# Kernel tuning notes

Hardware: AMD Instinct MI355X
Metric: run time of the kernel (lower is better)

Reference implementation:

```python
import jax, jax.numpy as jnp
import numpy as np
import math

LOG2PI = math.log(2.0 * math.pi)
NEG = -1e20


def gaussian_loglik(z, mean, log_std):
    tmp = (z - mean) * jnp.exp(-log_std)
    return -0.5 * (tmp * tmp + 2.0 * log_std + LOG2PI)


def setup_inputs() -> dict:
    key = jax.random.key(0)
    k1, k2 = jax.random.split(key)
    N, T, D = 16, 2048, 2
    # event arrival times, increasing along T
    input_time = jnp.sort(jax.random.uniform(k1, (N, T, 1), dtype=jnp.float32), axis=1)
    input_loc = jax.random.normal(k2, (N, T, D), dtype=jnp.float32)
    return {
        "input_time": input_time,
        "input_loc": input_loc,
        "mu0": jnp.asarray(0.0, jnp.float32),
        "logstd0": jnp.asarray(0.0, jnp.float32),
        "coeff_decay": jnp.asarray(0.1, jnp.float32),
        "spatial_logstd": jnp.asarray(0.1, jnp.float32),
    }


def reference(input_time, input_loc, mu0, logstd0, coeff_decay, spatial_logstd):
    N, T, _ = input_time.shape
    # base log-likelihood of the first event location under N(mu0, exp(logstd0))
    s0 = input_loc[:, 0]                                   # (N, D)
    loglik0 = gaussian_loglik(s0, mu0, logstd0).sum(-1)    # (N,)

    # pairwise time differences dt[n,i,j] = t[n,i] - t[n,j]
    dt = input_time - jnp.swapaxes(input_time, 1, 2)       # (N, T, T)

    # pairwise spatial Gaussian log-likelihoods, summed over D
    pw = gaussian_loglik(
        input_loc[:, :, None, :],                          # (N, T, 1, D)
        input_loc[:, None, :, :],                          # (N, 1, T, D)
        spatial_logstd,
    ).sum(-1)                                              # (N, T, T)

    # causal mask: keep strictly-lower triangle, fill rest with -1e20
    mask = jnp.tril(jnp.ones((T, T), dtype=bool), k=-1)
    pw = jnp.where(mask, pw, NEG)

    dt_logdecay = jnp.where(mask, -dt / jax.nn.softplus(coeff_decay), NEG)
    dt_logdecay = dt_logdecay - jax.nn.logsumexp(dt_logdecay, axis=-1, keepdims=True)

    loglik = jax.nn.logsumexp(pw + dt_logdecay, axis=-1)   # (N, T)
    return jnp.concatenate([loglik0[:, None], loglik[:, 1:]], axis=1)
```

## Files before the change

kernel.cpp:

```cpp
#include <hip/hip_runtime.h>
#include <math.h>

#define TT     2048
#define LOG2E  1.4426950408889634f
#define LN2    0.6931471805599453f
#define LOG2PI 1.8378770664093453f

__global__ __launch_bounds__(256) void gmsm_scan(
    const float* __restrict__ time,
    const float* __restrict__ loc,
    const float* __restrict__ coeffp,
    const float* __restrict__ lsp,
    float4* __restrict__ packed)
{
    const int n    = blockIdx.x;
    const int tid  = threadIdx.x;
    const int lane = tid & 63;
    const int wv   = tid >> 6;

    const float sp = log1pf(expf(*coeffp));
    const float ss = LOG2E / sp;
    const float ls = *lsp;
    const float c1 = -0.5f * expf(-2.0f * ls) * LOG2E;
    const float c0 = -(2.0f * ls + LOG2PI);

    const float4* tp = (const float4*)(time + (size_t)n * TT);
    const float4* lp = (const float4*)(loc  + (size_t)n * TT * 2);
    float4* pk = packed + (size_t)n * TT;

    const float4 t0 = tp[tid * 2 + 0];
    const float4 t1 = tp[tid * 2 + 1];
    const float4 l0 = lp[tid * 4 + 0];
    const float4 l1 = lp[tid * 4 + 1];
    const float4 l2 = lp[tid * 4 + 2];
    const float4 l3 = lp[tid * 4 + 3];

    const float tt[8] = {t0.x, t0.y, t0.z, t0.w, t1.x, t1.y, t1.z, t1.w};
    const float xx[8] = {l0.x, l0.z, l1.x, l1.z, l2.x, l2.z, l3.x, l3.z};
    const float yy[8] = {l0.y, l0.w, l1.y, l1.w, l2.y, l2.w, l3.y, l3.w};

    float bt[8], P[8];
    float run = 0.0f;
    #pragma unroll
    for (int k = 0; k < 8; ++k) {
        bt[k] = tt[k] * ss;
        run += __builtin_amdgcn_exp2f(bt[k]);
        P[k] = run;
    }
    const float tot = run;

    float v = tot;
    #pragma unroll
    for (int d = 1; d < 64; d <<= 1) {
        const float o = __shfl_up(v, d, 64);
        if (lane >= d) v += o;
    }
    __shared__ float wsum[4];
    if (lane == 63) wsum[wv] = v;
    __syncthreads();
    float excl = v - tot;
    for (int k = 0; k < wv; ++k) excl += wsum[k];

    #pragma unroll
    for (int k = 0; k < 8; ++k) {
        const int idx = tid * 8 + k;
        const float B = excl + (k ? P[k - 1] : 0.0f);
        const float r = fmaf(xx[k], xx[k], yy[k] * yy[k]);
        const float z = fmaf(r, c1, bt[k]);
        const float A = (idx == 0) ? 0.0f
            : fmaf(fmaf(r, c1, -__builtin_amdgcn_logf(B)), LN2, c0);
        pk[idx] = make_float4(xx[k], yy[k], z, A);
    }
}

__global__ __launch_bounds__(512) void gmsm_main(
    const float4* __restrict__ packed,
    const float* __restrict__ mu0p,
    const float* __restrict__ logstd0p,
    const float* __restrict__ lsp,
    float* __restrict__ out,
    int nrowblk)
{
    const int b    = blockIdx.x;
    const int half = nrowblk >> 1;
    const int g    = (b < half) ? (b << 1) : ((((nrowblk - 1) - b) << 1) | 1);
    const int n    = g >> 5;
    const int base = (g & 31) << 6;

    const int tid  = threadIdx.x;
    const int lane = tid & 63;
    const int w    = __builtin_amdgcn_readfirstlane(tid >> 6);

    const float4* __restrict__ pk = packed + (size_t)n * TT;

    const float ls   = *lsp;
    const float m2c1 = expf(-2.0f * ls) * LOG2E;
    const float4 pi  = pk[base + lane];
    const float u    = m2c1 * pi.x;
    const float v    = m2c1 * pi.y;

    float s = 0.0f;
    const int cfull = base >> 6;

    for (int c = w; c < cfull; c += 8) {
        const float4* cp = pk + (c << 6);
        #pragma unroll 8
        for (int jj = 0; jj < 64; ++jj) {
            const float4 f = cp[jj];
            s += __builtin_amdgcn_exp2f(fmaf(u, f.x, fmaf(v, f.y, f.z)));
        }
    }
    if (w == (cfull & 7)) {
        const float4* cp = pk + base;
        for (int jj = 0; jj < 63; ++jj) {
            const float4 f = cp[jj];
            const float e = __builtin_amdgcn_exp2f(fmaf(u, f.x, fmaf(v, f.y, f.z)));
            s += (jj < lane) ? e : 0.0f;
        }
    }

    __shared__ float lds[8 * 64];
    lds[tid] = s;
    __syncthreads();

    if (tid < 64) {
        float stot = 0.0f;
        #pragma unroll
        for (int k = 0; k < 8; ++k) stot += lds[(k << 6) | tid];
        const int i = base + tid;
        float res;
        if (i == 0) {
            const float mu0 = *mu0p, l0 = *logstd0p;
            const float inv = expf(-l0);
            const float4 p0 = pk[0];
            const float tx = (p0.x - mu0) * inv;
            const float ty = (p0.y - mu0) * inv;
            res = -0.5f * (tx * tx + ty * ty + 4.0f * l0 + 2.0f * LOG2PI);
        } else {
            const float A = pk[i].w;
            res = fmaf(__builtin_amdgcn_logf(stot), LN2, A);
        }
        out[(size_t)n * TT + i] = res;
    }
}

extern "C" void kernel_launch(void* const* d_in, const int* in_sizes, int n_in,
                              void* d_out, int out_size, void* d_ws, size_t ws_size,
                              hipStream_t stream) {
    const float* time   = (const float*)d_in[0];
    const float* loc    = (const float*)d_in[1];
    const float* mu0    = (const float*)d_in[2];
    const float* logstd = (const float*)d_in[3];
    const float* coeff  = (const float*)d_in[4];
    const float* sls    = (const float*)d_in[5];
    float* out = (float*)d_out;

    const int nrows = out_size;
    const int N     = nrows / TT;
    const int nrowblk = nrows >> 6;
    float4* packed = (float4*)d_ws;

    gmsm_scan<<<N, 256, 0, stream>>>(time, loc, coeff, sls, packed);
    gmsm_main<<<nrowblk, 512, 0, stream>>>(packed, mu0, logstd, sls, out, nrowblk);
}
```

Measured before the change: 78.44 us.

## Replace per-sequence prefix scan with elementwise pack and in-loop denominator sum

The first kernel no longer runs a block-wide prefix scan per sequence (one block per sequence, only 16 blocks). It becomes a fully parallel elementwise pack that stores exp2 of the scaled time in the w slot. The main kernel now accumulates that decay denominator alongside the spatial sum inside its existing pairwise loop, then combines the two logs at the end. This removes the low-parallelism scan launch at the cost of an extra add per pair, a second shared-memory reduction, and a second log.

```diff
diff --git a/kernel.cpp b/kernel.cpp
--- a/kernel.cpp
+++ b/kernel.cpp
@@ -6,71 +6,31 @@
 #define LN2    0.6931471805599453f
 #define LOG2PI 1.8378770664093453f
 
-__global__ __launch_bounds__(256) void gmsm_scan(
+__global__ __launch_bounds__(256) void gmsm_pack(
     const float* __restrict__ time,
     const float* __restrict__ loc,
     const float* __restrict__ coeffp,
     const float* __restrict__ lsp,
-    float4* __restrict__ packed)
+    float4* __restrict__ packed,
+    int total)
 {
-    const int n    = blockIdx.x;
-    const int tid  = threadIdx.x;
-    const int lane = tid & 63;
-    const int wv   = tid >> 6;
-
+    const int idx = blockIdx.x * 256 + threadIdx.x;
+    if (idx >= total) return;
     const float sp = log1pf(expf(*coeffp));
     const float ss = LOG2E / sp;
     const float ls = *lsp;
     const float c1 = -0.5f * expf(-2.0f * ls) * LOG2E;
-    const float c0 = -(2.0f * ls + LOG2PI);
 
-    const float4* tp = (const float4*)(time + (size_t)n * TT);
-    const float4* lp = (const float4*)(loc  + (size_t)n * TT * 2);
-    float4* pk = packed + (size_t)n * TT;
-
-    const float4 t0 = tp[tid * 2 + 0];
-    const float4 t1 = tp[tid * 2 + 1];
-    const float4 l0 = lp[tid * 4 + 0];
-    const float4 l1 = lp[tid * 4 + 1];
-    const float4 l2 = lp[tid * 4 + 2];
-    const float4 l3 = lp[tid * 4 + 3];
-
-    const float tt[8] = {t0.x, t0.y, t0.z, t0.w, t1.x, t1.y, t1.z, t1.w};
-    const float xx[8] = {l0.x, l0.z, l1.x, l1.z, l2.x, l2.z, l3.x, l3.z};
-    const float yy[8] = {l0.y, l0.w, l1.y, l1.w, l2.y, l2.w, l3.y, l3.w};
-
-    float bt[8], P[8];
-    float run = 0.0f;
-    #pragma unroll
-    for (int k = 0; k < 8; ++k) {
-        bt[k] = tt[k] * ss;
-        run += __builtin_amdgcn_exp2f(bt[k]);
-        P[k] = run;
-    }
-    const float tot = run;
-
-    float v = tot;
-    #pragma unroll
-    for (int d = 1; d < 64; d <<= 1) {
-        const float o = __shfl_up(v, d, 64);
-        if (lane >= d) v += o;
-    }
-    __shared__ float wsum[4];
-    if (lane == 63) wsum[wv] = v;
-    __syncthreads();
-    float excl = v - tot;
-    for (int k = 0; k < wv; ++k) excl += wsum[k];
-
-    #pragma unroll
-    for (int k = 0; k < 8; ++k) {
-        const int idx = tid * 8 + k;
-        const float B = excl + (k ? P[k - 1] : 0.0f);
-        const float r = fmaf(xx[k], xx[k], yy[k] * yy[k]);
-        const float z = fmaf(r, c1, bt[k]);
-        const float A = (idx == 0) ? 0.0f
-            : fmaf(fmaf(r, c1, -__builtin_amdgcn_logf(B)), LN2, c0);
-        pk[idx] = make_float4(xx[k], yy[k], z, A);
-    }
+    const float t   = time[idx];
+    const float2 xy = ((const float2*)loc)[idx];
+    const float bt  = t * ss;
+    const float r   = fmaf(xy.x, xy.x, xy.y * xy.y);
+    float4 o;
+    o.x = xy.x;
+    o.y = xy.y;
+    o.z = fmaf(r, c1, bt);
+    o.w = __builtin_amdgcn_exp2f(bt);
+    packed[idx] = o;
 }
 
 __global__ __launch_bounds__(512) void gmsm_main(
@@ -99,7 +59,8 @@
     const float u    = m2c1 * pi.x;
     const float v    = m2c1 * pi.y;
 
-    float s = 0.0f;
+    float s_q = 0.0f;
+    float s_b = 0.0f;
     const int cfull = base >> 6;
 
     for (int c = w; c < cfull; c += 8) {
@@ -107,7 +68,8 @@
         #pragma unroll 8
         for (int jj = 0; jj < 64; ++jj) {
             const float4 f = cp[jj];
-            s += __builtin_amdgcn_exp2f(fmaf(u, f.x, fmaf(v, f.y, f.z)));
+            s_q += __builtin_amdgcn_exp2f(fmaf(u, f.x, fmaf(v, f.y, f.z)));
+            s_b += f.w;
         }
     }
     if (w == (cfull & 7)) {
@@ -115,18 +77,25 @@
         for (int jj = 0; jj < 63; ++jj) {
             const float4 f = cp[jj];
             const float e = __builtin_amdgcn_exp2f(fmaf(u, f.x, fmaf(v, f.y, f.z)));
-            s += (jj < lane) ? e : 0.0f;
+            const bool on = jj < lane;
+            s_q += on ? e   : 0.0f;
+            s_b += on ? f.w : 0.0f;
         }
     }
 
-    __shared__ float lds[8 * 64];
-    lds[tid] = s;
+    __shared__ float ldsq[8 * 64];
+    __shared__ float ldsb[8 * 64];
+    ldsq[tid] = s_q;
+    ldsb[tid] = s_b;
     __syncthreads();
 
     if (tid < 64) {
-        float stot = 0.0f;
+        float q = 0.0f, bsum = 0.0f;
         #pragma unroll
-        for (int k = 0; k < 8; ++k) stot += lds[(k << 6) | tid];
+        for (int k = 0; k < 8; ++k) {
+            q    += ldsq[(k << 6) | tid];
+            bsum += ldsb[(k << 6) | tid];
+        }
         const int i = base + tid;
         float res;
         if (i == 0) {
@@ -137,8 +106,12 @@
             const float ty = (p0.y - mu0) * inv;
             res = -0.5f * (tx * tx + ty * ty + 4.0f * l0 + 2.0f * LOG2PI);
         } else {
-            const float A = pk[i].w;
-            res = fmaf(__builtin_amdgcn_logf(stot), LN2, A);
+            const float c1 = -0.5f * m2c1;
+            const float c0 = -(2.0f * ls + LOG2PI);
+            const float4 pr = pk[i];
+            const float r  = fmaf(pr.x, pr.x, pr.y * pr.y);
+            res = fmaf(__builtin_amdgcn_logf(q) - __builtin_amdgcn_logf(bsum)
+                       + c1 * r, LN2, c0);
         }
         out[(size_t)n * TT + i] = res;
     }
@@ -156,10 +129,10 @@
     float* out = (float*)d_out;
 
     const int nrows = out_size;
-    const int N     = nrows / TT;
     const int nrowblk = nrows >> 6;
     float4* packed = (float4*)d_ws;
 
-    gmsm_scan<<<N, 256, 0, stream>>>(time, loc, coeff, sls, packed);
+    gmsm_pack<<<(nrows + 255) / 256, 256, 0, stream>>>(time, loc, coeff, sls,
+                                                       packed, nrows);
     gmsm_main<<<nrowblk, 512, 0, stream>>>(packed, mu0, logstd, sls, out, nrowblk);
 }
```

Measured after the change: 79.52 us. Within noise of the previous version (+1.4%).
